# Kernel optimization log

Hardware: AMD Instinct MI355X
Metric: run time of the kernel (lower is better)

## Reference

```python
import jax, jax.numpy as jnp
import numpy as np

D_MODEL = 1024
N_HEADS = 16
D_KV = 64
B, S = 2, 2048


def setup_inputs() -> dict:
    key = jax.random.key(0)
    ks = jax.random.split(key, 7)
    scale = 1.0 / np.sqrt(D_MODEL)
    return {
        "query": jax.random.normal(ks[0], (B, S, D_MODEL), jnp.float32),
        "key": jax.random.normal(ks[1], (B, S, D_MODEL), jnp.float32),
        "value": jax.random.normal(ks[2], (B, S, D_MODEL), jnp.float32),
        "mask": jnp.zeros((B, 1, 1, S), jnp.float32),
        "Wq": jax.random.normal(ks[3], (D_MODEL, N_HEADS * D_KV), jnp.float32) * scale,
        "Wk": jax.random.normal(ks[4], (D_MODEL, N_HEADS * D_KV), jnp.float32) * scale,
        "Wv": jax.random.normal(ks[5], (D_MODEL, N_HEADS * D_KV), jnp.float32) * scale,
        "Wo": jax.random.normal(ks[6], (N_HEADS * D_KV, D_MODEL), jnp.float32) * scale,
    }


def _split_heads(x):
    b, s, _ = x.shape
    return x.reshape(b, s, N_HEADS, D_KV).transpose(0, 2, 1, 3)  # [B,H,S,Dk]


def reference(query, key, value, mask, Wq, Wk, Wv, Wo):
    q = _split_heads(query @ Wq)
    k = _split_heads(key @ Wk)
    v = _split_heads(value @ Wv)
    scores = jnp.einsum("bhqd,bhkd->bhqk", q, k) / jnp.sqrt(
        jnp.asarray(D_KV, scores_dtype := q.dtype)
    )
    scores = scores + mask
    attn = jax.nn.softmax(scores, axis=-1)  # dropout_rate=0 -> identity
    ctx = jnp.einsum("bhqk,bhkd->bhqd", attn, v)
    ctx = ctx.transpose(0, 2, 1, 3).reshape(query.shape[0], -1, N_HEADS * D_KV)
    hidden = ctx @ Wo
    return hidden
```

## Files before the change

### kernel.cpp

```cpp
#include <hip/hip_runtime.h>
#include <hip/hip_bf16.h>
#include <stdint.h>

typedef __bf16 bf16;
typedef __bf16 bf16x8 __attribute__((ext_vector_type(8)));
typedef __bf16 bf16x4 __attribute__((ext_vector_type(4)));
typedef float  f32x4  __attribute__((ext_vector_type(4)));
typedef float  f32x16 __attribute__((ext_vector_type(16)));

#define S_LEN  2048
#define NH     16
#define DKV    64
#define DMODEL 1024
#define LOG2E  1.4426950408889634f

#define SBAR()       __builtin_amdgcn_s_barrier()
#define SFENCE()     __builtin_amdgcn_sched_barrier(0)
#define WAIT_VM(N)   asm volatile("s_waitcnt vmcnt(" #N ")" ::: "memory")
#define WAIT_LGKM0() asm volatile("s_waitcnt lgkmcnt(0)" ::: "memory")

__device__ __forceinline__ void async_load16(const void* g, void* l) {
  __builtin_amdgcn_global_load_lds(
      (const __attribute__((address_space(1))) uint32_t*)(uintptr_t)g,
      (__attribute__((address_space(3))) uint32_t*)(uintptr_t)l,
      16, 0, 0);
}

__global__ void transpose_w(const float* __restrict__ W0, const float* __restrict__ W1,
                            const float* __restrict__ W2, const float* __restrict__ W3,
                            bf16* __restrict__ T0, bf16* __restrict__ T1,
                            bf16* __restrict__ T2, bf16* __restrict__ T3)
{
  int z = blockIdx.z;
  const float* W = (z == 0) ? W0 : (z == 1) ? W1 : (z == 2) ? W2 : W3;
  bf16* T = (z == 0) ? T0 : (z == 1) ? T1 : (z == 2) ? T2 : T3;
  __shared__ float tile[32][33];
  int n0 = blockIdx.x * 32, k0 = blockIdx.y * 32;
  int tx = threadIdx.x, ty = threadIdx.y;
  for (int i = 0; i < 32; i += 8)
    tile[ty + i][tx] = W[(size_t)(k0 + ty + i) * DMODEL + n0 + tx];
  __syncthreads();
  for (int i = 0; i < 32; i += 8)
    T[(size_t)(n0 + ty + i) * DMODEL + k0 + tx] = (bf16)tile[tx][ty + i];
}

__global__ __launch_bounds__(256) void gemm_qkv(
    const float* __restrict__ Aq, const float* __restrict__ Ak, const float* __restrict__ Av,
    const bf16* __restrict__ Bq, const bf16* __restrict__ Bk, const bf16* __restrict__ Bv,
    bf16* __restrict__ Cq, bf16* __restrict__ Ck, bf16* __restrict__ Cv)
{
  __shared__ __align__(16) char smem[49152];
  bf16* As  = (bf16*)smem;
  bf16* Bs0 = (bf16*)(smem + 16384);
  bf16* Bs1 = (bf16*)(smem + 32768);
  bf16* Ls  = (bf16*)smem;

  const int z = blockIdx.z;
  const float* A = (z == 0) ? Aq : (z == 1) ? Ak : Av;
  const bf16* Bt = (z == 0) ? Bq : (z == 1) ? Bk : Bv;
  bf16* C        = (z == 0) ? Cq : (z == 1) ? Ck : Cv;

  const int m0 = blockIdx.x * 128;
  const int n0 = blockIdx.y * 128;
  const int tid = threadIdx.x;
  const int lane = tid & 63;
  const int wave = tid >> 6;
  const int wm = (wave >> 1) * 64;
  const int wn = (wave & 1) * 64;
  const int row = lane & 15;
  const int quad = lane >> 4;

  f32x4 acc[4][4];
  for (int i = 0; i < 4; ++i)
    for (int j = 0; j < 4; ++j) acc[i][j] = (f32x4){0.f, 0.f, 0.f, 0.f};

  const int arc = tid & 7;
  const int arr = tid >> 3;
  const float* Ap0 = A + (size_t)(m0 +  0 + arr) * DMODEL + arc * 8;
  const float* Ap1 = A + (size_t)(m0 + 32 + arr) * DMODEL + arc * 8;
  const float* Ap2 = A + (size_t)(m0 + 64 + arr) * DMODEL + arc * 8;
  const float* Ap3 = A + (size_t)(m0 + 96 + arr) * DMODEL + arc * 8;

  auto stageB = [&](int kt, bf16* Bsel) {
    const int kk = kt << 6;
    for (int j = 0; j < 4; ++j) {
      int base = j * 256 + wave * 64;
      int idx = base + lane;
      int r = idx >> 3;
      int cc = (idx & 7) ^ (r & 7);
      async_load16(Bt + (size_t)(n0 + r) * DMODEL + kk + cc * 8,
                   (char*)Bsel + (size_t)base * 16);
    }
  };

  f32x4 av[4][2];
  av[0][0] = *(const f32x4*)(Ap0); av[0][1] = *(const f32x4*)(Ap0 + 4);
  av[1][0] = *(const f32x4*)(Ap1); av[1][1] = *(const f32x4*)(Ap1 + 4);
  av[2][0] = *(const f32x4*)(Ap2); av[2][1] = *(const f32x4*)(Ap2 + 4);
  av[3][0] = *(const f32x4*)(Ap3); av[3][1] = *(const f32x4*)(Ap3 + 4);
  SFENCE();
  stageB(0, Bs0);
  SFENCE();

  for (int kt = 0; kt < 16; ++kt) {
    bf16* Bcur = (kt & 1) ? Bs1 : Bs0;
    bf16* Bnxt = (kt & 1) ? Bs0 : Bs1;
    if (kt < 15) stageB(kt + 1, Bnxt);
#pragma unroll
    for (int g = 0; g < 4; ++g) {
      bf16x8 o;
      for (int w = 0; w < 4; ++w) { o[w] = (bf16)av[g][0][w]; o[w + 4] = (bf16)av[g][1][w]; }
      int r = g * 32 + arr;
      *(bf16x8*)(As + r * 64 + ((arc ^ (arr & 7)) << 3)) = o;
    }
    if (kt < 15) {
      const int kn = (kt + 1) << 6;
      av[0][0] = *(const f32x4*)(Ap0 + kn); av[0][1] = *(const f32x4*)(Ap0 + kn + 4);
      av[1][0] = *(const f32x4*)(Ap1 + kn); av[1][1] = *(const f32x4*)(Ap1 + kn + 4);
      av[2][0] = *(const f32x4*)(Ap2 + kn); av[2][1] = *(const f32x4*)(Ap2 + kn + 4);
      av[3][0] = *(const f32x4*)(Ap3 + kn); av[3][1] = *(const f32x4*)(Ap3 + kn + 4);
    }
    SFENCE();
    if (kt < 15) { WAIT_VM(12); }
    else         { WAIT_VM(0); }
    WAIT_LGKM0();
    SBAR();
    SFENCE();
    for (int ks = 0; ks < 2; ++ks) {
      bf16x8 af[4], bfr[4];
      for (int i = 0; i < 4; ++i) {
        int rr = wm + i * 16 + row;
        af[i] = *(const bf16x8*)(As + rr * 64 + (((quad + ks * 4) ^ (rr & 7)) << 3));
      }
      for (int j = 0; j < 4; ++j) {
        int rr = wn + j * 16 + row;
        bfr[j] = *(const bf16x8*)(Bcur + rr * 64 + (((quad + ks * 4) ^ (rr & 7)) << 3));
      }
      for (int i = 0; i < 4; ++i)
        for (int j = 0; j < 4; ++j)
          acc[i][j] = __builtin_amdgcn_mfma_f32_16x16x32_bf16(af[i], bfr[j], acc[i][j], 0, 0, 0);
    }
    SFENCE();
    SBAR();
  }

  if (z != 2) {
    const int bq = m0 >> 11;
    __syncthreads();
    for (int i = 0; i < 4; ++i)
      for (int j = 0; j < 4; ++j)
        for (int r = 0; r < 4; ++r)
          Ls[(wm + i * 16 + quad * 4 + r) * 132 + wn + j * 16 + row] = (bf16)acc[i][j][r];
    __syncthreads();
    for (int u = 0; u < 8; ++u) {
      int cc = u * 256 + tid;
      int rloc = cc >> 4, c8 = (cc & 15) * 8;
      int s = (m0 + rloc) & 2047;
      int gn = n0 + c8;
      int h = gn >> 6, d = gn & 63;
      bf16x8 val = *(const bf16x8*)(Ls + rloc * 132 + c8);
      *(bf16x8*)(C + (((size_t)(bq * NH + h)) * S_LEN + s) * DKV + d) = val;
    }
  } else {
    for (int i = 0; i < 4; ++i)
      for (int j = 0; j < 4; ++j) {
        int gm = m0 + wm + i * 16 + quad * 4;
        int gn = n0 + wn + j * 16 + row;
        int b = gm >> 11, s = gm & 2047;
        int h = gn >> 6,  d = gn & 63;
        int bh = b * NH + h;
        int tile = s >> 6, kb = (s & 63) >> 2;
        bf16x4 t;
        for (int r = 0; r < 4; ++r) t[r] = (bf16)acc[i][j][r];
        *(bf16x4*)(C + ((((size_t)bh * 32 + tile) * 16 + kb) * 64 + d) * 4) = t;
      }
  }
}

__global__ __launch_bounds__(256, 4) void attn_kernel(
    const bf16* __restrict__ Qh, const bf16* __restrict__ Kh, const bf16* __restrict__ Vperm,
    const float* __restrict__ mask, bf16* __restrict__ Opart, float* __restrict__ Lpart)
{
  __shared__ __align__(16) bf16 Ks[2][64 * 64];
  __shared__ __align__(16) bf16 Vts[2][64 * 64];
  __shared__ __align__(16) float masks2[2][64];

  const int bh = blockIdx.x;
  const int b = bh >> 4;
  const int q0 = blockIdx.y * 128;
  const int zh = blockIdx.z;
  const int tid = threadIdx.x;
  const int lane = tid & 63;
  const int wave = tid >> 6;
  const int ln = lane & 31;
  const int hi = lane >> 5;
  const float SC2 = 0.125f * LOG2E;

  const int qg = q0 + wave * 32 + ln;
  bf16x8 qf[4];
  {
    const bf16* qrow = Qh + ((size_t)bh * S_LEN + qg) * DKV;
    for (int c = 0; c < 4; ++c)
      qf[c] = *(const bf16x8*)(qrow + c * 16 + hi * 8);
  }

  auto stage = [&](int it, int buf) {
    const int kv0 = zh * 1024 + it * 64;
    float mval = 0.f;
    if (tid < 64) mval = mask[b * S_LEN + kv0 + tid];
    const bf16* vtile = Vperm + ((size_t)bh * 32 + (kv0 >> 6)) * 4096;
    for (int j = 0; j < 2; ++j) {
      int base = j * 256 + wave * 64;
      int idx = base + lane;
      int r = idx >> 3;
      int cc = (idx & 7) ^ (r & 7);
      async_load16(Kh + ((size_t)bh * S_LEN + kv0 + r) * DKV + cc * 8,
                   (char*)Ks[buf] + (size_t)base * 16);
      async_load16(vtile + (size_t)idx * 8,
                   (char*)Vts[buf] + (size_t)base * 16);
    }
    if (tid < 64) masks2[buf][tid] = mval * LOG2E;
  };

  f32x16 O[2];
  for (int nb = 0; nb < 2; ++nb)
    for (int i = 0; i < 16; ++i) O[nb][i] = 0.f;
  float lsum = 0.f;

  stage(0, 0);

  for (int it = 0; it < 16; ++it) {
    const int cur = it & 1;
    if (it < 15) stage(it + 1, cur ^ 1);
    SFENCE();
    if (it < 15) { WAIT_VM(4); }
    else         { WAIT_VM(0); }
    WAIT_LGKM0();
    SBAR();
    SFENCE();

    f32x16 Sm[2];
    for (int i = 0; i < 16; ++i) { Sm[0][i] = 0.f; Sm[1][i] = 0.f; }
    for (int c = 0; c < 4; ++c) {
      bf16x8 k0 = *(const bf16x8*)(Ks[cur] + ln * 64        + (((2 * c + hi) ^ (ln & 7)) << 3));
      bf16x8 k1 = *(const bf16x8*)(Ks[cur] + (32 + ln) * 64 + (((2 * c + hi) ^ (ln & 7)) << 3));
      Sm[0] = __builtin_amdgcn_mfma_f32_32x32x16_bf16(k0, qf[c], Sm[0], 0, 0, 0);
      Sm[1] = __builtin_amdgcn_mfma_f32_32x32x16_bf16(k1, qf[c], Sm[1], 0, 0, 0);
    }

    for (int cg = 0; cg < 4; ++cg) {
      int mb = cg >> 1, g = cg & 1;
      int koff = 32 * mb + 16 * g + 4 * hi;
      f32x4 mklo = *(const f32x4*)(&masks2[cur][koff]);
      f32x4 mkhi = *(const f32x4*)(&masks2[cur][koff + 8]);
      bf16x8 ap;
      float ls0 = 0.f;
      for (int u = 0; u < 4; ++u) {
        float p = __builtin_amdgcn_exp2f(Sm[mb][g * 8 + u] * SC2 + mklo[u]);
        ls0 += p; ap[u] = (bf16)p;
      }
      for (int u = 0; u < 4; ++u) {
        float p = __builtin_amdgcn_exp2f(Sm[mb][g * 8 + 4 + u] * SC2 + mkhi[u]);
        ls0 += p; ap[4 + u] = (bf16)p;
      }
      lsum += ls0;
      int kb0 = hi + 4 * g + 8 * mb;
      for (int nb = 0; nb < 2; ++nb) {
        int d = nb * 32 + ln;
        bf16x4 lo = *(const bf16x4*)(Vts[cur] + ((size_t)kb0 * 64 + d) * 4);
        bf16x4 hv = *(const bf16x4*)(Vts[cur] + ((size_t)(kb0 + 2) * 64 + d) * 4);
        bf16x8 bv;
        for (int u = 0; u < 4; ++u) { bv[u] = lo[u]; bv[u + 4] = hv[u]; }
        O[nb] = __builtin_amdgcn_mfma_f32_32x32x16_bf16(ap, bv, O[nb], 0, 0, 0);
      }
    }
    SFENCE();
    SBAR();
  }

  float lt = lsum + __shfl_xor(lsum, 32, 64);
  if (lane < 32)
    Lpart[((size_t)zh * 32 + bh) * S_LEN + q0 + wave * 32 + ln] = lt;

  bf16* ob = Opart + (((size_t)zh * 32 + bh) * S_LEN) * DKV;
  for (int g = 0; g < 4; ++g)
    for (int nb = 0; nb < 2; ++nb)
      for (int j = 0; j < 4; ++j) {
        int qrow = q0 + wave * 32 + j + 8 * g + 4 * hi;
        ob[(size_t)qrow * DKV + nb * 32 + ln] = (bf16)O[nb][g * 4 + j];
      }
}

__global__ __launch_bounds__(256) void gemm_out(
    const bf16* __restrict__ Opart, const float* __restrict__ Lpart,
    const bf16* __restrict__ Wot, float* __restrict__ Cout)
{
  __shared__ __align__(16) bf16 As[32 * 64];
  __shared__ __align__(16) bf16 Bs[2][128 * 64];
  __shared__ float rinv[NH * 32];

  const int m0 = blockIdx.x * 32;
  const int n0 = blockIdx.y * 128;
  const int tid = threadIdx.x;
  const int lane = tid & 63;
  const int wave = tid >> 6;
  const int wm = (wave >> 1) * 16;
  const int wn = (wave & 1) * 64;
  const int row = lane & 15;
  const int quad = lane >> 4;
  const int b = m0 >> 11;
  const int s0 = m0 & 2047;

  for (int u = 0; u < 2; ++u) {
    int idx = u * 256 + tid;
    int h = idx >> 5, r = idx & 31;
    float l = Lpart[((size_t)(b * NH + h)) * S_LEN + s0 + r]
            + Lpart[((size_t)(32 + b * NH + h)) * S_LEN + s0 + r];
    rinv[idx] = 1.0f / l;
  }

  f32x4 acc[4];
  for (int j = 0; j < 4; ++j) acc[j] = (f32x4){0.f, 0.f, 0.f, 0.f};

  const int arc = tid & 7;
  const int arr = tid >> 3;
  const bf16* O0p = Opart + ((size_t)(b * NH) * S_LEN + s0 + arr) * DKV + arc * 8;
  const bf16* O1p = Opart + ((size_t)(32 + b * NH) * S_LEN + s0 + arr) * DKV + arc * 8;
  const size_t HSTEP = (size_t)S_LEN * DKV;

  auto stageB = [&](int kt, int buf) {
    for (int j = 0; j < 4; ++j) {
      int base = j * 256 + wave * 64;
      int idx = base + lane;
      int r = idx >> 3;
      int cc = (idx & 7) ^ (r & 7);
      async_load16(Wot + (size_t)(n0 + r) * DMODEL + kt * 64 + cc * 8,
                   (char*)Bs[buf] + (size_t)base * 16);
    }
  };

  stageB(0, 0);
  bf16x8 h0 = *(const bf16x8*)(O0p);
  bf16x8 h1 = *(const bf16x8*)(O1p);
  WAIT_LGKM0();
  SBAR();

  for (int kt = 0; kt < 16; ++kt) {
    const int cur = kt & 1;
    if (kt < 15) stageB(kt + 1, cur ^ 1);
    {
      float rv = rinv[kt * 32 + arr];
      bf16x8 o;
      for (int w = 0; w < 8; ++w)
        o[w] = (bf16)(((float)h0[w] + (float)h1[w]) * rv);
      *(bf16x8*)(As + arr * 64 + ((arc ^ (arr & 7)) << 3)) = o;
    }
    if (kt < 15) {
      h0 = *(const bf16x8*)(O0p + (size_t)(kt + 1) * HSTEP);
      h1 = *(const bf16x8*)(O1p + (size_t)(kt + 1) * HSTEP);
    }
    SFENCE();
    if (kt < 15) { WAIT_VM(6); }
    else         { WAIT_VM(0); }
    WAIT_LGKM0();
    SBAR();
    SFENCE();
    for (int ks = 0; ks < 2; ++ks) {
      bf16x8 af, bfr[4];
      {
        int rr = wm + row;
        af = *(const bf16x8*)(As + rr * 64 + (((quad + ks * 4) ^ (rr & 7)) << 3));
      }
      for (int j = 0; j < 4; ++j) {
        int rr = wn + j * 16 + row;
        bfr[j] = *(const bf16x8*)(Bs[cur] + rr * 64 + (((quad + ks * 4) ^ (rr & 7)) << 3));
      }
      for (int j = 0; j < 4; ++j)
        acc[j] = __builtin_amdgcn_mfma_f32_16x16x32_bf16(af, bfr[j], acc[j], 0, 0, 0);
    }
    SFENCE();
    SBAR();
  }

  for (int j = 0; j < 4; ++j)
    for (int r = 0; r < 4; ++r) {
      int gm = m0 + wm + quad * 4 + r;
      int gn = n0 + wn + j * 16 + row;
      Cout[(size_t)gm * DMODEL + gn] = acc[j][r];
    }
}

extern "C" void kernel_launch(void* const* d_in, const int* in_sizes, int n_in,
                              void* d_out, int out_size, void* d_ws, size_t ws_size,
                              hipStream_t stream)
{
  const float* query = (const float*)d_in[0];
  const float* key_  = (const float*)d_in[1];
  const float* value = (const float*)d_in[2];
  const float* mask  = (const float*)d_in[3];
  const float* Wq = (const float*)d_in[4];
  const float* Wk = (const float*)d_in[5];
  const float* Wv = (const float*)d_in[6];
  const float* Wo = (const float*)d_in[7];

  char* ws = (char*)d_ws;
  const size_t MB = (size_t)1 << 20;
  bf16* qh    = (bf16*)(ws + 0 * MB);
  bf16* kh    = (bf16*)(ws + 8 * MB);
  bf16* vperm = (bf16*)(ws + 16 * MB);
  bf16* wot   = (bf16*)(ws + 24 * MB);
  bf16* Opart = (bf16*)(ws + 26 * MB);
  bf16* wqt   = (bf16*)(ws + 26 * MB);
  bf16* wkt   = (bf16*)(ws + 28 * MB);
  bf16* wvt   = (bf16*)(ws + 30 * MB);
  float* Lpart = (float*)(ws + 58 * MB);

  transpose_w<<<dim3(32, 32, 4), dim3(32, 8), 0, stream>>>(Wq, Wk, Wv, Wo, wqt, wkt, wvt, wot);
  gemm_qkv<<<dim3(32, 8, 3), 256, 0, stream>>>(query, key_, value, wqt, wkt, wvt,
                                               qh, kh, vperm);
  attn_kernel<<<dim3(32, 16, 2), 256, 0, stream>>>(qh, kh, vperm, mask, Opart, Lpart);
  gemm_out<<<dim3(128, 8), 256, 0, stream>>>(Opart, Lpart, wot, (float*)d_out);
}
```

Baseline: 208.7 us.

## Widen weight transpose tiles, repack V for 8-wide loads, enlarge out-proj tile

The weight transpose kernel now uses 64x64 tiles, reading with vectorized float4 loads and writing 8 bf16 values at a time. The V permutation layout is changed so attention can fetch each MFMA B operand with one 16-byte LDS read instead of two 8-byte reads plus a shuffle. The first QK MFMA now takes a zero register directly instead of re-zeroing the accumulator every iteration. The output GEMM doubles its M tile to 64 rows per block to reuse the Wo tiles more, at the cost of fewer blocks and more registers.

New measurement: 225.4 us. +8.0%, slower.

```diff
diff --git a/kernel.cpp b/kernel.cpp
--- a/kernel.cpp
+++ b/kernel.cpp
@@ -34,14 +34,27 @@
   int z = blockIdx.z;
   const float* W = (z == 0) ? W0 : (z == 1) ? W1 : (z == 2) ? W2 : W3;
   bf16* T = (z == 0) ? T0 : (z == 1) ? T1 : (z == 2) ? T2 : T3;
-  __shared__ float tile[32][33];
-  int n0 = blockIdx.x * 32, k0 = blockIdx.y * 32;
-  int tx = threadIdx.x, ty = threadIdx.y;
-  for (int i = 0; i < 32; i += 8)
-    tile[ty + i][tx] = W[(size_t)(k0 + ty + i) * DMODEL + n0 + tx];
+  __shared__ float tile[64][65];
+  int n0 = blockIdx.x * 64, k0 = blockIdx.y * 64;
+  int tid = threadIdx.x;
+
+  int c4 = (tid & 15) * 4;
+  int rr = tid >> 4;
+  for (int g = 0; g < 4; ++g) {
+    int k = g * 16 + rr;
+    f32x4 v = *(const f32x4*)(W + (size_t)(k0 + k) * DMODEL + n0 + c4);
+    tile[k][c4] = v[0]; tile[k][c4 + 1] = v[1];
+    tile[k][c4 + 2] = v[2]; tile[k][c4 + 3] = v[3];
+  }
   __syncthreads();
-  for (int i = 0; i < 32; i += 8)
-    T[(size_t)(n0 + ty + i) * DMODEL + k0 + tx] = (bf16)tile[tx][ty + i];
+
+  int kc = tid & 7, rn2 = tid >> 3;
+  for (int pass = 0; pass < 2; ++pass) {
+    int rn = pass * 32 + rn2;
+    bf16x8 o;
+    for (int w = 0; w < 8; ++w) o[w] = (bf16)tile[kc * 8 + w][rn];
+    *(bf16x8*)(T + (size_t)(n0 + rn) * DMODEL + k0 + kc * 8) = o;
+  }
 }
 
 __global__ __launch_bounds__(256) void gemm_qkv(
@@ -170,9 +183,11 @@
         int h = gn >> 6,  d = gn & 63;
         int bh = b * NH + h;
         int tile = s >> 6, kb = (s & 63) >> 2;
+        int half = (kb >> 1) & 1;
+        int p = (kb & 1) + ((kb >> 2) & 1) * 2 + (kb >> 3) * 4;
         bf16x4 t;
         for (int r = 0; r < 4; ++r) t[r] = (bf16)acc[i][j][r];
-        *(bf16x4*)(C + ((((size_t)bh * 32 + tile) * 16 + kb) * 64 + d) * 4) = t;
+        *(bf16x4*)(C + ((((size_t)bh * 32 + tile) * 8 + p) * 64 + d) * 8 + half * 4) = t;
       }
   }
 }
@@ -195,6 +210,11 @@
   const int ln = lane & 31;
   const int hi = lane >> 5;
   const float SC2 = 0.125f * LOG2E;
+
+  float zseed;
+  asm volatile("v_mov_b32 %0, 0" : "=v"(zseed));
+  f32x16 z16;
+  for (int i = 0; i < 16; ++i) z16[i] = zseed;
 
   const int qg = q0 + wave * 32 + ln;
   bf16x8 qf[4];
@@ -240,8 +260,13 @@
     SFENCE();
 
     f32x16 Sm[2];
-    for (int i = 0; i < 16; ++i) { Sm[0][i] = 0.f; Sm[1][i] = 0.f; }
-    for (int c = 0; c < 4; ++c) {
+    {
+      bf16x8 k0 = *(const bf16x8*)(Ks[cur] + ln * 64        + ((hi ^ (ln & 7)) << 3));
+      bf16x8 k1 = *(const bf16x8*)(Ks[cur] + (32 + ln) * 64 + ((hi ^ (ln & 7)) << 3));
+      Sm[0] = __builtin_amdgcn_mfma_f32_32x32x16_bf16(k0, qf[0], z16, 0, 0, 0);
+      Sm[1] = __builtin_amdgcn_mfma_f32_32x32x16_bf16(k1, qf[0], z16, 0, 0, 0);
+    }
+    for (int c = 1; c < 4; ++c) {
       bf16x8 k0 = *(const bf16x8*)(Ks[cur] + ln * 64        + (((2 * c + hi) ^ (ln & 7)) << 3));
       bf16x8 k1 = *(const bf16x8*)(Ks[cur] + (32 + ln) * 64 + (((2 * c + hi) ^ (ln & 7)) << 3));
       Sm[0] = __builtin_amdgcn_mfma_f32_32x32x16_bf16(k0, qf[c], Sm[0], 0, 0, 0);
@@ -264,13 +289,10 @@
         ls0 += p; ap[4 + u] = (bf16)p;
       }
       lsum += ls0;
-      int kb0 = hi + 4 * g + 8 * mb;
+      int p = hi + 2 * g + 4 * mb;
       for (int nb = 0; nb < 2; ++nb) {
         int d = nb * 32 + ln;
-        bf16x4 lo = *(const bf16x4*)(Vts[cur] + ((size_t)kb0 * 64 + d) * 4);
-        bf16x4 hv = *(const bf16x4*)(Vts[cur] + ((size_t)(kb0 + 2) * 64 + d) * 4);
-        bf16x8 bv;
-        for (int u = 0; u < 4; ++u) { bv[u] = lo[u]; bv[u + 4] = hv[u]; }
+        bf16x8 bv = *(const bf16x8*)(Vts[cur] + ((size_t)p * 64 + d) * 8);
         O[nb] = __builtin_amdgcn_mfma_f32_32x32x16_bf16(ap, bv, O[nb], 0, 0, 0);
       }
     }
@@ -295,38 +317,41 @@
     const bf16* __restrict__ Opart, const float* __restrict__ Lpart,
     const bf16* __restrict__ Wot, float* __restrict__ Cout)
 {
-  __shared__ __align__(16) bf16 As[32 * 64];
+  __shared__ __align__(16) bf16 As[64 * 64];
   __shared__ __align__(16) bf16 Bs[2][128 * 64];
-  __shared__ float rinv[NH * 32];
-
-  const int m0 = blockIdx.x * 32;
+  __shared__ float rinv[NH * 64];
+
+  const int m0 = blockIdx.x * 64;
   const int n0 = blockIdx.y * 128;
   const int tid = threadIdx.x;
   const int lane = tid & 63;
   const int wave = tid >> 6;
-  const int wm = (wave >> 1) * 16;
+  const int wm = (wave >> 1) * 32;
   const int wn = (wave & 1) * 64;
   const int row = lane & 15;
   const int quad = lane >> 4;
   const int b = m0 >> 11;
   const int s0 = m0 & 2047;
 
-  for (int u = 0; u < 2; ++u) {
+  for (int u = 0; u < 4; ++u) {
     int idx = u * 256 + tid;
-    int h = idx >> 5, r = idx & 31;
-    float l = Lpart[((size_t)(b * NH + h)) * S_LEN + s0 + r]
-            + Lpart[((size_t)(32 + b * NH + h)) * S_LEN + s0 + r];
+    int h = idx >> 6, r = idx & 63;
+    float l = Lpart[(size_t)(b * NH + h) * S_LEN + s0 + r]
+            + Lpart[(size_t)(32 + b * NH + h) * S_LEN + s0 + r];
     rinv[idx] = 1.0f / l;
   }
-
-  f32x4 acc[4];
-  for (int j = 0; j < 4; ++j) acc[j] = (f32x4){0.f, 0.f, 0.f, 0.f};
+  SFENCE();
+
+  f32x4 acc[2][4];
+  for (int i = 0; i < 2; ++i)
+    for (int j = 0; j < 4; ++j) acc[i][j] = (f32x4){0.f, 0.f, 0.f, 0.f};
 
   const int arc = tid & 7;
   const int arr = tid >> 3;
-  const bf16* O0p = Opart + ((size_t)(b * NH) * S_LEN + s0 + arr) * DKV + arc * 8;
-  const bf16* O1p = Opart + ((size_t)(32 + b * NH) * S_LEN + s0 + arr) * DKV + arc * 8;
   const size_t HSTEP = (size_t)S_LEN * DKV;
+  const size_t ZSTEP = (size_t)32 * S_LEN * DKV;
+  const bf16* Oa = Opart + ((size_t)(b * NH) * S_LEN + s0 + arr) * DKV + arc * 8;
+  const bf16* Ob = Oa + (size_t)32 * DKV;
 
   auto stageB = [&](int kt, int buf) {
     for (int j = 0; j < 4; ++j) {
@@ -339,9 +364,13 @@
     }
   };
 
+  bf16x8 h00 = *(const bf16x8*)(Oa);
+  bf16x8 h01 = *(const bf16x8*)(Oa + ZSTEP);
+  bf16x8 h10 = *(const bf16x8*)(Ob);
+  bf16x8 h11 = *(const bf16x8*)(Ob + ZSTEP);
+  SFENCE();
   stageB(0, 0);
-  bf16x8 h0 = *(const bf16x8*)(O0p);
-  bf16x8 h1 = *(const bf16x8*)(O1p);
+  SFENCE();
   WAIT_LGKM0();
   SBAR();
 
@@ -349,45 +378,54 @@
     const int cur = kt & 1;
     if (kt < 15) stageB(kt + 1, cur ^ 1);
     {
-      float rv = rinv[kt * 32 + arr];
+      float rv  = rinv[kt * 64 + arr];
+      float rv2 = rinv[kt * 64 + 32 + arr];
       bf16x8 o;
       for (int w = 0; w < 8; ++w)
-        o[w] = (bf16)(((float)h0[w] + (float)h1[w]) * rv);
+        o[w] = (bf16)(((float)h00[w] + (float)h01[w]) * rv);
       *(bf16x8*)(As + arr * 64 + ((arc ^ (arr & 7)) << 3)) = o;
+      for (int w = 0; w < 8; ++w)
+        o[w] = (bf16)(((float)h10[w] + (float)h11[w]) * rv2);
+      *(bf16x8*)(As + (32 + arr) * 64 + ((arc ^ (arr & 7)) << 3)) = o;
     }
     if (kt < 15) {
-      h0 = *(const bf16x8*)(O0p + (size_t)(kt + 1) * HSTEP);
-      h1 = *(const bf16x8*)(O1p + (size_t)(kt + 1) * HSTEP);
-    }
-    SFENCE();
-    if (kt < 15) { WAIT_VM(6); }
+      const size_t off = (size_t)(kt + 1) * HSTEP;
+      h00 = *(const bf16x8*)(Oa + off);
+      h01 = *(const bf16x8*)(Oa + off + ZSTEP);
+      h10 = *(const bf16x8*)(Ob + off);
+      h11 = *(const bf16x8*)(Ob + off + ZSTEP);
+    }
+    SFENCE();
+    if (kt < 15) { WAIT_VM(8); }
     else         { WAIT_VM(0); }
     WAIT_LGKM0();
     SBAR();
     SFENCE();
     for (int ks = 0; ks < 2; ++ks) {
-      bf16x8 af, bfr[4];
-      {
-        int rr = wm + row;
-        af = *(const bf16x8*)(As + rr * 64 + (((quad + ks * 4) ^ (rr & 7)) << 3));
+      bf16x8 af[2], bfr[4];
+      for (int i = 0; i < 2; ++i) {
+        int rr = wm + i * 16 + row;
+        af[i] = *(const bf16x8*)(As + rr * 64 + (((quad + ks * 4) ^ (rr & 7)) << 3));
       }
       for (int j = 0; j < 4; ++j) {
         int rr = wn + j * 16 + row;
         bfr[j] = *(const bf16x8*)(Bs[cur] + rr * 64 + (((quad + ks * 4) ^ (rr & 7)) << 3));
       }
-      for (int j = 0; j < 4; ++j)
-        acc[j] = __builtin_amdgcn_mfma_f32_16x16x32_bf16(af, bfr[j], acc[j], 0, 0, 0);
-    }
-    SFENCE();
-    SBAR();
-  }
-
-  for (int j = 0; j < 4; ++j)
-    for (int r = 0; r < 4; ++r) {
-      int gm = m0 + wm + quad * 4 + r;
-      int gn = n0 + wn + j * 16 + row;
-      Cout[(size_t)gm * DMODEL + gn] = acc[j][r];
-    }
+      for (int i = 0; i < 2; ++i)
+        for (int j = 0; j < 4; ++j)
+          acc[i][j] = __builtin_amdgcn_mfma_f32_16x16x32_bf16(af[i], bfr[j], acc[i][j], 0, 0, 0);
+    }
+    SFENCE();
+    SBAR();
+  }
+
+  for (int i = 0; i < 2; ++i)
+    for (int j = 0; j < 4; ++j)
+      for (int r = 0; r < 4; ++r) {
+        int gm = m0 + wm + i * 16 + quad * 4 + r;
+        int gn = n0 + wn + j * 16 + row;
+        Cout[(size_t)gm * DMODEL + gn] = acc[i][j][r];
+      }
 }
 
 extern "C" void kernel_launch(void* const* d_in, const int* in_sizes, int n_in,
@@ -415,9 +453,9 @@
   bf16* wvt   = (bf16*)(ws + 30 * MB);
   float* Lpart = (float*)(ws + 58 * MB);
 
-  transpose_w<<<dim3(32, 32, 4), dim3(32, 8), 0, stream>>>(Wq, Wk, Wv, Wo, wqt, wkt, wvt, wot);
+  transpose_w<<<dim3(16, 16, 4), 256, 0, stream>>>(Wq, Wk, Wv, Wo, wqt, wkt, wvt, wot);
   gemm_qkv<<<dim3(32, 8, 3), 256, 0, stream>>>(query, key_, value, wqt, wkt, wvt,
                                                qh, kh, vperm);
   attn_kernel<<<dim3(32, 16, 2), 256, 0, stream>>>(qh, kh, vperm, mask, Opart, Lpart);
-  gemm_out<<<dim3(128, 8), 256, 0, stream>>>(Opart, Lpart, wot, (float*)d_out);
-}
+  gemm_out<<<dim3(64, 8), 256, 0, stream>>>(Opart, Lpart, wot, (float*)d_out);
+}
```
